# Kernel optimization log

Measured on AMD Instinct MI355X. Metric: run time of the kernel, lower is better.

## Reference

```python
import jax, jax.numpy as jnp
import numpy as np

N_SRC = 100000
N_DST = 20000
E = 1250000
D_IN = 64
D_OUT = 64
NEG_SLOPE = 0.2  # PyG GATConv default


def setup_inputs() -> dict:
    key = jax.random.key(0)
    ks = jax.random.split(key, 8)
    x = jax.random.normal(ks[0], (N_SRC, D_IN), dtype=jnp.float32)
    res_n_id = jax.random.randint(ks[1], (N_DST,), 0, N_SRC)
    edge_src = jax.random.randint(ks[2], (E,), 0, N_SRC)
    edge_dst = jax.random.randint(ks[3], (E,), 0, N_DST)
    W = jax.random.normal(ks[4], (D_IN, D_OUT), dtype=jnp.float32) / np.sqrt(D_IN)
    att_src = jax.random.normal(ks[5], (D_OUT,), dtype=jnp.float32)
    att_dst = jax.random.normal(ks[6], (D_OUT,), dtype=jnp.float32)
    bias = jax.random.normal(ks[7], (D_OUT,), dtype=jnp.float32) * 0.01
    return {"x": x, "res_n_id": res_n_id, "edge_src": edge_src,
            "edge_dst": edge_dst, "W": W, "att_src": att_src,
            "att_dst": att_dst, "bias": bias}


def reference(x, res_n_id, edge_src, edge_dst, W, att_src, att_dst, bias):
    # Shared linear transform (in_channels is an int -> one weight in PyG)
    h_src = x @ W                      # [N_src, D_OUT]
    h_dst = x[res_n_id] @ W            # [N_dst, D_OUT]
    # Per-node attention logits
    a_src = h_src @ att_src            # [N_src]
    a_dst = h_dst @ att_dst            # [N_dst]
    # Per-edge attention score (gather)
    e = jax.nn.leaky_relu(a_src[edge_src] + a_dst[edge_dst], NEG_SLOPE)  # [E]
    # Segment softmax over incoming edges of each destination node
    m = jax.ops.segment_max(e, edge_dst, num_segments=N_DST)             # [N_dst]
    ex = jnp.exp(e - m[edge_dst])
    denom = jax.ops.segment_sum(ex, edge_dst, num_segments=N_DST)        # [N_dst]
    alpha = ex / (denom[edge_dst] + 1e-16)                               # [E]
    # (dropout on alpha is eval-mode identity)
    # Weighted scatter-aggregate
    msg = h_src[edge_src] * alpha[:, None]                               # [E, D_OUT]
    out = jax.ops.segment_sum(msg, edge_dst, num_segments=N_DST)         # [N_dst, D_OUT]
    return out + bias
```

## Files before the change

### kernel.cpp

```cpp
#include <hip/hip_runtime.h>

#define N_SRC 100000
#define N_DST 20000
#define NE    1250000
#define D     64
#define NEG_SLOPE 0.2f

#define NBKT 1250
#define BCAP 1536
#define TILE 4096

__device__ __forceinline__ unsigned short f2bf(float f) {
    unsigned u = __float_as_uint(f);
    u += 0x7FFFu + ((u >> 16) & 1);
    return (unsigned short)(u >> 16);
}
__device__ __forceinline__ float blo(unsigned u) { return __uint_as_float(u << 16); }
__device__ __forceinline__ float bhi(unsigned u) { return __uint_as_float(u & 0xFFFF0000u); }

__global__ void k_wad_init(const float* __restrict__ W,
                           const float* __restrict__ att_dst,
                           float* __restrict__ wad, int* __restrict__ gcur) {
    int g = blockIdx.x * 256 + threadIdx.x;
    if (g < NBKT) gcur[g] = g * BCAP;
    if (g < D) {
        float s = 0.f;
#pragma unroll
        for (int c = 0; c < D; ++c) s += W[g * D + c] * att_dst[c];
        wad[g] = s;
    }
}

__global__ __launch_bounds__(256) void k_h(const float* __restrict__ x,
                                           const float* __restrict__ W,
                                           const float* __restrict__ att_src,
                                           unsigned short* __restrict__ hb,
                                           float* __restrict__ a_src) {
    __shared__ float xs[64 * 68];
    __shared__ float Ws[64 * 64];
    int t = threadIdx.x;
    int row0 = blockIdx.x * 64;
    int nrows = N_SRC - row0; if (nrows > 64) nrows = 64;
    {
        const float4* W4 = (const float4*)W;
        float4* Ws4 = (float4*)Ws;
#pragma unroll
        for (int p = 0; p < 4; ++p) Ws4[t + 256 * p] = W4[t + 256 * p];
    }
#pragma unroll
    for (int p = 0; p < 4; ++p) {
        int idx = t + 256 * p;
        int r = idx >> 4, kq = idx & 15;
        float4 v = make_float4(0.f, 0.f, 0.f, 0.f);
        if (r < nrows) v = *(const float4*)(x + (size_t)(row0 + r) * D + 4 * kq);
        xs[(4 * kq + 0) * 68 + r] = v.x;
        xs[(4 * kq + 1) * 68 + r] = v.y;
        xs[(4 * kq + 2) * 68 + r] = v.z;
        xs[(4 * kq + 3) * 68 + r] = v.w;
    }
    __syncthreads();
    int ry = t >> 4, cx = t & 15;
    float acc[4][4] = {{0.f}};
#pragma unroll 8
    for (int k = 0; k < 64; ++k) {
        float4 xv = *(const float4*)(xs + k * 68 + 4 * ry);
        float4 wv = *(const float4*)(Ws + k * 64 + 4 * cx);
        acc[0][0] = fmaf(xv.x, wv.x, acc[0][0]); acc[0][1] = fmaf(xv.x, wv.y, acc[0][1]);
        acc[0][2] = fmaf(xv.x, wv.z, acc[0][2]); acc[0][3] = fmaf(xv.x, wv.w, acc[0][3]);
        acc[1][0] = fmaf(xv.y, wv.x, acc[1][0]); acc[1][1] = fmaf(xv.y, wv.y, acc[1][1]);
        acc[1][2] = fmaf(xv.y, wv.z, acc[1][2]); acc[1][3] = fmaf(xv.y, wv.w, acc[1][3]);
        acc[2][0] = fmaf(xv.z, wv.x, acc[2][0]); acc[2][1] = fmaf(xv.z, wv.y, acc[2][1]);
        acc[2][2] = fmaf(xv.z, wv.z, acc[2][2]); acc[2][3] = fmaf(xv.z, wv.w, acc[2][3]);
        acc[3][0] = fmaf(xv.w, wv.x, acc[3][0]); acc[3][1] = fmaf(xv.w, wv.y, acc[3][1]);
        acc[3][2] = fmaf(xv.w, wv.z, acc[3][2]); acc[3][3] = fmaf(xv.w, wv.w, acc[3][3]);
    }
    float4 a4 = *(const float4*)(att_src + 4 * cx);
#pragma unroll
    for (int j = 0; j < 4; ++j) {
        int r = 4 * ry + j;
        if (r < nrows) {
            ushort4 hv;
            hv.x = f2bf(acc[j][0]); hv.y = f2bf(acc[j][1]);
            hv.z = f2bf(acc[j][2]); hv.w = f2bf(acc[j][3]);
            *(ushort4*)(hb + (size_t)(row0 + r) * D + 4 * cx) = hv;
        }
        float p = acc[j][0] * a4.x + acc[j][1] * a4.y + acc[j][2] * a4.z + acc[j][3] * a4.w;
        p += __shfl_xor(p, 1, 64); p += __shfl_xor(p, 2, 64);
        p += __shfl_xor(p, 4, 64); p += __shfl_xor(p, 8, 64);
        if (cx == 0 && r < nrows) a_src[row0 + r] = p;
    }
}

__global__ __launch_bounds__(256) void k_adst(const float* __restrict__ x,
                                              const int* __restrict__ res_n_id,
                                              const float* __restrict__ wad,
                                              float* __restrict__ a_dst) {
    int tid = threadIdx.x;
    int wid = blockIdx.x * 4 + (tid >> 6);
    int lane = tid & 63;
    if (wid >= N_DST) return;
    int row = res_n_id[wid];
    float p = x[(size_t)row * D + lane] * wad[lane];
#pragma unroll
    for (int off = 32; off; off >>= 1) p += __shfl_xor(p, off, 64);
    if (lane == 0) a_dst[wid] = p;
}

__global__ __launch_bounds__(1024) void k_bucket(const int* __restrict__ es,
                                                 const int* __restrict__ ed,
                                                 int* __restrict__ gcur,
                                                 int* __restrict__ buf) {
    __shared__ int hist[NBKT];
    __shared__ int lofs[NBKT];
    __shared__ int gbase[NBKT];
    __shared__ int wtot[16];
    __shared__ int stage[TILE];
    int t = threadIdx.x;
    int w = t >> 6, lane = t & 63;
    int base = blockIdx.x * TILE;
    int nE = NE - base; if (nE > TILE) nE = TILE;

    for (int i = t; i < NBKT; i += 1024) hist[i] = 0;
    __syncthreads();

    int s_[4], d_[4], rk_[4];
#pragma unroll
    for (int j = 0; j < 4; ++j) {
        int i = t + 1024 * j;
        d_[j] = -1;
        if (i < nE) {
            s_[j] = es[base + i];
            d_[j] = ed[base + i];
            rk_[j] = atomicAdd(&hist[d_[j] >> 4], 1);
        }
    }
    __syncthreads();

    int c0 = t * 2;
    int h0 = 0, h1 = 0;
    if (c0 < NBKT) { h0 = hist[c0]; h1 = hist[c0 + 1]; }
    int sum = h0 + h1;
    int incl = sum;
#pragma unroll
    for (int off = 1; off < 64; off <<= 1) {
        int u = __shfl_up(incl, off, 64);
        if (lane >= off) incl += u;
    }
    if (lane == 63) wtot[w] = incl;
    __syncthreads();
    int wpre = 0;
#pragma unroll
    for (int j = 0; j < 16; ++j) wpre += (j < w) ? wtot[j] : 0;
    if (c0 < NBKT) {
        int run = wpre + incl - sum;
        lofs[c0] = run;
        gbase[c0] = h0 ? atomicAdd(&gcur[c0], h0) : 0;
        run += h0;
        lofs[c0 + 1] = run;
        gbase[c0 + 1] = h1 ? atomicAdd(&gcur[c0 + 1], h1) : 0;
    }
    __syncthreads();

#pragma unroll
    for (int j = 0; j < 4; ++j) {
        if (d_[j] >= 0) {
            int b = d_[j] >> 4;
            stage[lofs[b] + rk_[j]] = s_[j] | ((d_[j] & 15) << 17) | (b << 21);
        }
    }
    __syncthreads();

    for (int idx = t; idx < nE; idx += 1024) {
        int rec = stage[idx];
        int b = ((unsigned)rec) >> 21;
        int gpos = gbase[b] + idx - lofs[b];
        if (gpos < (b + 1) * BCAP) buf[gpos] = rec;
    }
}

__global__ __launch_bounds__(512) void k_aggB(const int* __restrict__ buf,
                                              const int* __restrict__ gcur,
                                              const float* __restrict__ a_src,
                                              const float* __restrict__ a_dst,
                                              const unsigned short* __restrict__ hb,
                                              const float* __restrict__ bias,
                                              float* __restrict__ out) {
    __shared__ int2 sorted[BCAP];
    __shared__ int  scw[16 * 8];
    __shared__ int  begs[17];
    int bk = blockIdx.x;
    int t = threadIdx.x;
    int w = t >> 6, lane = t & 63;
    int n = gcur[bk] - bk * BCAP;
    if (n > BCAP) n = BCAP;
    if (n < 0) n = 0;

    const int* src = buf + (size_t)bk * BCAP;
    int r0 = 0, r1 = 0, r2 = 0;
    int bin0 = -1, bin1 = -1, bin2 = -1;
    if (t < n)        { r0 = src[t];        bin0 = (r0 >> 17) & 15; }
    if (t + 512 < n)  { r1 = src[t + 512];  bin1 = (r1 >> 17) & 15; }
    if (t + 1024 < n) { r2 = src[t + 1024]; bin2 = (r2 >> 17) & 15; }

    int h[16], incl[16];
#pragma unroll
    for (int i = 0; i < 16; ++i)
        h[i] = (bin0 == i) + (bin1 == i) + (bin2 == i);

#pragma unroll
    for (int i = 0; i < 16; ++i) {
        int v = h[i];
#pragma unroll
        for (int off = 1; off < 64; off <<= 1) {
            int u = __shfl_up(v, off, 64);
            if (lane >= off) v += u;
        }
        incl[i] = v;
        int tot = __shfl(v, 63, 64);
        if (lane == 0) scw[i * 8 + w] = tot;
    }
    __syncthreads();

    for (int off = 1; off < 128; off <<= 1) {
        int up = 0;
        if (t < 128 && t >= off) up = scw[t - off];
        __syncthreads();
        if (t < 128 && t >= off) scw[t] += up;
        __syncthreads();
    }
    if (t < 16) begs[t] = (t == 0) ? 0 : scw[t * 8 - 1];
    if (t == 16) begs[16] = n;

    int p0 = 0, p1 = 0, p2 = 0;
#pragma unroll
    for (int i = 0; i < 16; ++i) {
        int idx = i * 8 + w;
        int base_i = ((idx ? scw[idx - 1] : 0)) + (incl[i] - h[i]);
        p0 += (bin0 == i) ? base_i : 0;
        p1 += (bin1 == i) ? base_i : 0;
        p2 += (bin2 == i) ? base_i : 0;
    }
    p1 += (bin1 == bin0);
    p2 += (bin2 == bin0) + (bin2 == bin1);
    if (bin0 >= 0) sorted[p0].x = r0;
    if (bin1 >= 0) sorted[p1].x = r1;
    if (bin2 >= 0) sorted[p2].x = r2;
    __syncthreads();

    int g = lane >> 3, il = lane & 7;
    float4 bA = *(const float4*)(bias + 8 * il);
    float4 bB = *(const float4*)(bias + 8 * il + 4);
#pragma unroll
    for (int q = 0; q < 2; ++q) {
        int dlo = w * 2 + q;
        int beg = begs[dlo], end = begs[dlo + 1];
        float ad = a_dst[bk * 16 + dlo];

        float mx = -1e30f;
        for (int i = beg + lane; i < end; i += 64) {
            int meta = sorted[i].x;
            float v = a_src[meta & 0x1FFFF] + ad;
            v = v > 0.f ? v : NEG_SLOPE * v;
            sorted[i].y = __float_as_int(v);
            mx = fmaxf(mx, v);
        }
#pragma unroll
        for (int off = 32; off; off >>= 1) mx = fmaxf(mx, __shfl_xor(mx, off, 64));
        __builtin_amdgcn_wave_barrier();

        float a0 = 0.f, a1 = 0.f, a2 = 0.f, a3 = 0.f;
        float a4c = 0.f, a5 = 0.f, a6 = 0.f, a7 = 0.f;
        float den = 0.f;
        int i = beg;
        for (; i + 16 <= end; i += 16) {
            int2 ra = sorted[i + g];
            int2 rb = sorted[i + 8 + g];
            const uint4 ha = *(const uint4*)(hb + (size_t)(ra.x & 0x1FFFF) * D + 8 * il);
            const uint4 hc = *(const uint4*)(hb + (size_t)(rb.x & 0x1FFFF) * D + 8 * il);
            float ea = __expf(__int_as_float(ra.y) - mx);
            float eb = __expf(__int_as_float(rb.y) - mx);
            a0 = fmaf(ea, blo(ha.x), a0); a1 = fmaf(ea, bhi(ha.x), a1);
            a2 = fmaf(ea, blo(ha.y), a2); a3 = fmaf(ea, bhi(ha.y), a3);
            a4c = fmaf(ea, blo(ha.z), a4c); a5 = fmaf(ea, bhi(ha.z), a5);
            a6 = fmaf(ea, blo(ha.w), a6); a7 = fmaf(ea, bhi(ha.w), a7);
            a0 = fmaf(eb, blo(hc.x), a0); a1 = fmaf(eb, bhi(hc.x), a1);
            a2 = fmaf(eb, blo(hc.y), a2); a3 = fmaf(eb, bhi(hc.y), a3);
            a4c = fmaf(eb, blo(hc.z), a4c); a5 = fmaf(eb, bhi(hc.z), a5);
            a6 = fmaf(eb, blo(hc.w), a6); a7 = fmaf(eb, bhi(hc.w), a7);
            den += ea + eb;
        }
        for (; i < end; i += 8) {
            int idx = i + g;
            bool ok = idx < end;
            float e = 0.f;
            if (ok) {
                int2 r = sorted[idx];
                e = __expf(__int_as_float(r.y) - mx);
                const uint4 hv = *(const uint4*)(hb + (size_t)(r.x & 0x1FFFF) * D + 8 * il);
                a0 = fmaf(e, blo(hv.x), a0); a1 = fmaf(e, bhi(hv.x), a1);
                a2 = fmaf(e, blo(hv.y), a2); a3 = fmaf(e, bhi(hv.y), a3);
                a4c = fmaf(e, blo(hv.z), a4c); a5 = fmaf(e, bhi(hv.z), a5);
                a6 = fmaf(e, blo(hv.w), a6); a7 = fmaf(e, bhi(hv.w), a7);
            }
            den += e;
        }
#pragma unroll
        for (int off = 8; off <= 32; off <<= 1) {
            a0 += __shfl_xor(a0, off, 64); a1 += __shfl_xor(a1, off, 64);
            a2 += __shfl_xor(a2, off, 64); a3 += __shfl_xor(a3, off, 64);
            a4c += __shfl_xor(a4c, off, 64); a5 += __shfl_xor(a5, off, 64);
            a6 += __shfl_xor(a6, off, 64); a7 += __shfl_xor(a7, off, 64);
            den += __shfl_xor(den, off, 64);
        }
        if (g == 0) {
            float inv = 1.f / (den + 1e-16f);
            float4 oA, oB;
            oA.x = a0 * inv + bA.x; oA.y = a1 * inv + bA.y;
            oA.z = a2 * inv + bA.z; oA.w = a3 * inv + bA.w;
            oB.x = a4c * inv + bB.x; oB.y = a5 * inv + bB.y;
            oB.z = a6 * inv + bB.z; oB.w = a7 * inv + bB.w;
            float* orow = out + ((size_t)bk * 16 + dlo) * D + 8 * il;
            *(float4*)orow = oA;
            *(float4*)(orow + 4) = oB;
        }
    }
}

extern "C" void kernel_launch(void* const* d_in, const int* in_sizes, int n_in,
                              void* d_out, int out_size, void* d_ws, size_t ws_size,
                              hipStream_t stream) {
    const float* x        = (const float*)d_in[0];
    const int*   res_n_id = (const int*)d_in[1];
    const int*   edge_src = (const int*)d_in[2];
    const int*   edge_dst = (const int*)d_in[3];
    const float* W        = (const float*)d_in[4];
    const float* att_src  = (const float*)d_in[5];
    const float* att_dst  = (const float*)d_in[6];
    const float* bias     = (const float*)d_in[7];
    float* out = (float*)d_out;

    char* w = (char*)d_ws;
    unsigned short* hb = (unsigned short*)w; w += (size_t)N_SRC * D * 2;
    int*   buf   = (int*)w;   w += (size_t)NBKT * BCAP * 4;
    float* a_src = (float*)w; w += (size_t)N_SRC * 4;
    float* a_dst = (float*)w; w += (size_t)N_DST * 4;
    float* wad   = (float*)w; w += 256;
    int*   gcur  = (int*)w;   w += (size_t)NBKT * 4;

    k_wad_init<<<(NBKT + 255) / 256, 256, 0, stream>>>(W, att_dst, wad, gcur);
    k_h<<<(N_SRC + 63) / 64, 256, 0, stream>>>(x, W, att_src, hb, a_src);
    k_adst<<<N_DST / 4, 256, 0, stream>>>(x, res_n_id, wad, a_dst);
    k_bucket<<<(NE + TILE - 1) / TILE, 1024, 0, stream>>>(edge_src, edge_dst, gcur, buf);
    k_aggB<<<NBKT, 512, 0, stream>>>(buf, gcur, a_src, a_dst, hb, bias, out);
}
```

Measured before the change: 168.3 us.

## Halve bucket size, fuse a_dst computation into aggregation, unroll gather by four

Buckets now hold 8 destination nodes instead of 16 (2500 buckets, capacity 768), and the aggregation kernel runs with 256 threads per block. The separate a_dst kernel is removed; each wave computes its destination's attention logit inline from x, res_n_id and wad, which saves one launch and one global round-trip. The block-level scan now uses a single-wave shuffle scan instead of a multi-barrier shared-memory scan. A 32-edge unrolled loop adds more independent gathers in flight, at the cost of more registers and smaller per-bucket capacity margins for overflow.

Measured after the change: 161.3 us. 4.2% less time.

```diff
diff --git a/kernel.cpp b/kernel.cpp
--- a/kernel.cpp
+++ b/kernel.cpp
@@ -6,8 +6,8 @@
 #define D     64
 #define NEG_SLOPE 0.2f
 
-#define NBKT 1250
-#define BCAP 1536
+#define NBKT 2500
+#define BCAP 768
 #define TILE 4096
 
 __device__ __forceinline__ unsigned short f2bf(float f) {
@@ -91,21 +91,6 @@
     }
 }
 
-__global__ __launch_bounds__(256) void k_adst(const float* __restrict__ x,
-                                              const int* __restrict__ res_n_id,
-                                              const float* __restrict__ wad,
-                                              float* __restrict__ a_dst) {
-    int tid = threadIdx.x;
-    int wid = blockIdx.x * 4 + (tid >> 6);
-    int lane = tid & 63;
-    if (wid >= N_DST) return;
-    int row = res_n_id[wid];
-    float p = x[(size_t)row * D + lane] * wad[lane];
-#pragma unroll
-    for (int off = 32; off; off >>= 1) p += __shfl_xor(p, off, 64);
-    if (lane == 0) a_dst[wid] = p;
-}
-
 __global__ __launch_bounds__(1024) void k_bucket(const int* __restrict__ es,
                                                  const int* __restrict__ ed,
                                                  int* __restrict__ gcur,
@@ -131,15 +116,17 @@
         if (i < nE) {
             s_[j] = es[base + i];
             d_[j] = ed[base + i];
-            rk_[j] = atomicAdd(&hist[d_[j] >> 4], 1);
-        }
-    }
-    __syncthreads();
-
-    int c0 = t * 2;
-    int h0 = 0, h1 = 0;
-    if (c0 < NBKT) { h0 = hist[c0]; h1 = hist[c0 + 1]; }
-    int sum = h0 + h1;
+            rk_[j] = atomicAdd(&hist[d_[j] >> 3], 1);
+        }
+    }
+    __syncthreads();
+
+    int c0 = t * 3;
+    int hc[3] = {0, 0, 0};
+#pragma unroll
+    for (int j = 0; j < 3; ++j)
+        if (c0 + j < NBKT) hc[j] = hist[c0 + j];
+    int sum = hc[0] + hc[1] + hc[2];
     int incl = sum;
 #pragma unroll
     for (int off = 1; off < 64; off <<= 1) {
@@ -151,43 +138,49 @@
     int wpre = 0;
 #pragma unroll
     for (int j = 0; j < 16; ++j) wpre += (j < w) ? wtot[j] : 0;
-    if (c0 < NBKT) {
+    {
         int run = wpre + incl - sum;
-        lofs[c0] = run;
-        gbase[c0] = h0 ? atomicAdd(&gcur[c0], h0) : 0;
-        run += h0;
-        lofs[c0 + 1] = run;
-        gbase[c0 + 1] = h1 ? atomicAdd(&gcur[c0 + 1], h1) : 0;
+#pragma unroll
+        for (int j = 0; j < 3; ++j) {
+            int b = c0 + j;
+            if (b < NBKT) {
+                lofs[b] = run;
+                gbase[b] = hc[j] ? atomicAdd(&gcur[b], hc[j]) : 0;
+                run += hc[j];
+            }
+        }
     }
     __syncthreads();
 
 #pragma unroll
     for (int j = 0; j < 4; ++j) {
         if (d_[j] >= 0) {
-            int b = d_[j] >> 4;
-            stage[lofs[b] + rk_[j]] = s_[j] | ((d_[j] & 15) << 17) | (b << 21);
+            int b = d_[j] >> 3;
+            stage[lofs[b] + rk_[j]] = s_[j] | ((d_[j] & 7) << 17) | (b << 20);
         }
     }
     __syncthreads();
 
     for (int idx = t; idx < nE; idx += 1024) {
         int rec = stage[idx];
-        int b = ((unsigned)rec) >> 21;
+        int b = ((unsigned)rec) >> 20;
         int gpos = gbase[b] + idx - lofs[b];
         if (gpos < (b + 1) * BCAP) buf[gpos] = rec;
     }
 }
 
-__global__ __launch_bounds__(512) void k_aggB(const int* __restrict__ buf,
+__global__ __launch_bounds__(256) void k_aggB(const int* __restrict__ buf,
                                               const int* __restrict__ gcur,
                                               const float* __restrict__ a_src,
-                                              const float* __restrict__ a_dst,
+                                              const float* __restrict__ x,
+                                              const int* __restrict__ res_n_id,
+                                              const float* __restrict__ wad,
                                               const unsigned short* __restrict__ hb,
                                               const float* __restrict__ bias,
                                               float* __restrict__ out) {
     __shared__ int2 sorted[BCAP];
-    __shared__ int  scw[16 * 8];
-    __shared__ int  begs[17];
+    __shared__ int  scw[8 * 4];
+    __shared__ int  begs[9];
     int bk = blockIdx.x;
     int t = threadIdx.x;
     int w = t >> 6, lane = t & 63;
@@ -198,17 +191,17 @@
     const int* src = buf + (size_t)bk * BCAP;
     int r0 = 0, r1 = 0, r2 = 0;
     int bin0 = -1, bin1 = -1, bin2 = -1;
-    if (t < n)        { r0 = src[t];        bin0 = (r0 >> 17) & 15; }
-    if (t + 512 < n)  { r1 = src[t + 512];  bin1 = (r1 >> 17) & 15; }
-    if (t + 1024 < n) { r2 = src[t + 1024]; bin2 = (r2 >> 17) & 15; }
-
-    int h[16], incl[16];
-#pragma unroll
-    for (int i = 0; i < 16; ++i)
+    if (t < n)       { r0 = src[t];       bin0 = (r0 >> 17) & 7; }
+    if (t + 256 < n) { r1 = src[t + 256]; bin1 = (r1 >> 17) & 7; }
+    if (t + 512 < n) { r2 = src[t + 512]; bin2 = (r2 >> 17) & 7; }
+
+    int h[8], incl[8];
+#pragma unroll
+    for (int i = 0; i < 8; ++i)
         h[i] = (bin0 == i) + (bin1 == i) + (bin2 == i);
 
 #pragma unroll
-    for (int i = 0; i < 16; ++i) {
+    for (int i = 0; i < 8; ++i) {
         int v = h[i];
 #pragma unroll
         for (int off = 1; off < 64; off <<= 1) {
@@ -217,24 +210,27 @@
         }
         incl[i] = v;
         int tot = __shfl(v, 63, 64);
-        if (lane == 0) scw[i * 8 + w] = tot;
-    }
-    __syncthreads();
-
-    for (int off = 1; off < 128; off <<= 1) {
-        int up = 0;
-        if (t < 128 && t >= off) up = scw[t - off];
-        __syncthreads();
-        if (t < 128 && t >= off) scw[t] += up;
-        __syncthreads();
-    }
-    if (t < 16) begs[t] = (t == 0) ? 0 : scw[t * 8 - 1];
-    if (t == 16) begs[16] = n;
+        if (lane == 0) scw[i * 4 + w] = tot;
+    }
+    __syncthreads();
+
+    if (t < 32) {
+        int v = scw[t];
+#pragma unroll
+        for (int off = 1; off < 32; off <<= 1) {
+            int u = __shfl_up(v, off, 64);
+            if (t >= off) v += u;
+        }
+        scw[t] = v;
+    }
+    __syncthreads();
+    if (t < 8) begs[t] = (t == 0) ? 0 : scw[t * 4 - 1];
+    if (t == 8) begs[8] = n;
 
     int p0 = 0, p1 = 0, p2 = 0;
 #pragma unroll
-    for (int i = 0; i < 16; ++i) {
-        int idx = i * 8 + w;
+    for (int i = 0; i < 8; ++i) {
+        int idx = i * 4 + w;
         int base_i = ((idx ? scw[idx - 1] : 0)) + (incl[i] - h[i]);
         p0 += (bin0 == i) ? base_i : 0;
         p1 += (bin1 == i) ? base_i : 0;
@@ -245,6 +241,7 @@
     if (bin0 >= 0) sorted[p0].x = r0;
     if (bin1 >= 0) sorted[p1].x = r1;
     if (bin2 >= 0) sorted[p2].x = r2;
+    float wv = wad[lane];
     __syncthreads();
 
     int g = lane >> 3, il = lane & 7;
@@ -254,7 +251,11 @@
     for (int q = 0; q < 2; ++q) {
         int dlo = w * 2 + q;
         int beg = begs[dlo], end = begs[dlo + 1];
-        float ad = a_dst[bk * 16 + dlo];
+
+        int xrow = res_n_id[bk * 8 + dlo];
+        float ad = x[(size_t)xrow * D + lane] * wv;
+#pragma unroll
+        for (int off = 32; off; off >>= 1) ad += __shfl_xor(ad, off, 64);
 
         float mx = -1e30f;
         for (int i = beg + lane; i < end; i += 64) {
@@ -272,21 +273,52 @@
         float a4c = 0.f, a5 = 0.f, a6 = 0.f, a7 = 0.f;
         float den = 0.f;
         int i = beg;
+        for (; i + 32 <= end; i += 32) {
+            int2 ra = sorted[i + g];
+            int2 rb = sorted[i + 8 + g];
+            int2 rc = sorted[i + 16 + g];
+            int2 rd = sorted[i + 24 + g];
+            const uint4 ha = *(const uint4*)(hb + (size_t)(ra.x & 0x1FFFF) * D + 8 * il);
+            const uint4 hc4 = *(const uint4*)(hb + (size_t)(rb.x & 0x1FFFF) * D + 8 * il);
+            const uint4 he = *(const uint4*)(hb + (size_t)(rc.x & 0x1FFFF) * D + 8 * il);
+            const uint4 hf = *(const uint4*)(hb + (size_t)(rd.x & 0x1FFFF) * D + 8 * il);
+            float ea = __expf(__int_as_float(ra.y) - mx);
+            float eb = __expf(__int_as_float(rb.y) - mx);
+            float ec = __expf(__int_as_float(rc.y) - mx);
+            float ed = __expf(__int_as_float(rd.y) - mx);
+            a0 = fmaf(ea, blo(ha.x), a0); a1 = fmaf(ea, bhi(ha.x), a1);
+            a2 = fmaf(ea, blo(ha.y), a2); a3 = fmaf(ea, bhi(ha.y), a3);
+            a4c = fmaf(ea, blo(ha.z), a4c); a5 = fmaf(ea, bhi(ha.z), a5);
+            a6 = fmaf(ea, blo(ha.w), a6); a7 = fmaf(ea, bhi(ha.w), a7);
+            a0 = fmaf(eb, blo(hc4.x), a0); a1 = fmaf(eb, bhi(hc4.x), a1);
+            a2 = fmaf(eb, blo(hc4.y), a2); a3 = fmaf(eb, bhi(hc4.y), a3);
+            a4c = fmaf(eb, blo(hc4.z), a4c); a5 = fmaf(eb, bhi(hc4.z), a5);
+            a6 = fmaf(eb, blo(hc4.w), a6); a7 = fmaf(eb, bhi(hc4.w), a7);
+            a0 = fmaf(ec, blo(he.x), a0); a1 = fmaf(ec, bhi(he.x), a1);
+            a2 = fmaf(ec, blo(he.y), a2); a3 = fmaf(ec, bhi(he.y), a3);
+            a4c = fmaf(ec, blo(he.z), a4c); a5 = fmaf(ec, bhi(he.z), a5);
+            a6 = fmaf(ec, blo(he.w), a6); a7 = fmaf(ec, bhi(he.w), a7);
+            a0 = fmaf(ed, blo(hf.x), a0); a1 = fmaf(ed, bhi(hf.x), a1);
+            a2 = fmaf(ed, blo(hf.y), a2); a3 = fmaf(ed, bhi(hf.y), a3);
+            a4c = fmaf(ed, blo(hf.z), a4c); a5 = fmaf(ed, bhi(hf.z), a5);
+            a6 = fmaf(ed, blo(hf.w), a6); a7 = fmaf(ed, bhi(hf.w), a7);
+            den += (ea + eb) + (ec + ed);
+        }
         for (; i + 16 <= end; i += 16) {
             int2 ra = sorted[i + g];
             int2 rb = sorted[i + 8 + g];
             const uint4 ha = *(const uint4*)(hb + (size_t)(ra.x & 0x1FFFF) * D + 8 * il);
-            const uint4 hc = *(const uint4*)(hb + (size_t)(rb.x & 0x1FFFF) * D + 8 * il);
+            const uint4 hc4 = *(const uint4*)(hb + (size_t)(rb.x & 0x1FFFF) * D + 8 * il);
             float ea = __expf(__int_as_float(ra.y) - mx);
             float eb = __expf(__int_as_float(rb.y) - mx);
             a0 = fmaf(ea, blo(ha.x), a0); a1 = fmaf(ea, bhi(ha.x), a1);
             a2 = fmaf(ea, blo(ha.y), a2); a3 = fmaf(ea, bhi(ha.y), a3);
             a4c = fmaf(ea, blo(ha.z), a4c); a5 = fmaf(ea, bhi(ha.z), a5);
             a6 = fmaf(ea, blo(ha.w), a6); a7 = fmaf(ea, bhi(ha.w), a7);
-            a0 = fmaf(eb, blo(hc.x), a0); a1 = fmaf(eb, bhi(hc.x), a1);
-            a2 = fmaf(eb, blo(hc.y), a2); a3 = fmaf(eb, bhi(hc.y), a3);
-            a4c = fmaf(eb, blo(hc.z), a4c); a5 = fmaf(eb, bhi(hc.z), a5);
-            a6 = fmaf(eb, blo(hc.w), a6); a7 = fmaf(eb, bhi(hc.w), a7);
+            a0 = fmaf(eb, blo(hc4.x), a0); a1 = fmaf(eb, bhi(hc4.x), a1);
+            a2 = fmaf(eb, blo(hc4.y), a2); a3 = fmaf(eb, bhi(hc4.y), a3);
+            a4c = fmaf(eb, blo(hc4.z), a4c); a5 = fmaf(eb, bhi(hc4.z), a5);
+            a6 = fmaf(eb, blo(hc4.w), a6); a7 = fmaf(eb, bhi(hc4.w), a7);
             den += ea + eb;
         }
         for (; i < end; i += 8) {
@@ -319,7 +351,7 @@
             oA.z = a2 * inv + bA.z; oA.w = a3 * inv + bA.w;
             oB.x = a4c * inv + bB.x; oB.y = a5 * inv + bB.y;
             oB.z = a6 * inv + bB.z; oB.w = a7 * inv + bB.w;
-            float* orow = out + ((size_t)bk * 16 + dlo) * D + 8 * il;
+            float* orow = out + ((size_t)bk * 8 + dlo) * D + 8 * il;
             *(float4*)orow = oA;
             *(float4*)(orow + 4) = oB;
         }
@@ -343,13 +375,11 @@
     unsigned short* hb = (unsigned short*)w; w += (size_t)N_SRC * D * 2;
     int*   buf   = (int*)w;   w += (size_t)NBKT * BCAP * 4;
     float* a_src = (float*)w; w += (size_t)N_SRC * 4;
-    float* a_dst = (float*)w; w += (size_t)N_DST * 4;
     float* wad   = (float*)w; w += 256;
     int*   gcur  = (int*)w;   w += (size_t)NBKT * 4;
 
     k_wad_init<<<(NBKT + 255) / 256, 256, 0, stream>>>(W, att_dst, wad, gcur);
     k_h<<<(N_SRC + 63) / 64, 256, 0, stream>>>(x, W, att_src, hb, a_src);
-    k_adst<<<N_DST / 4, 256, 0, stream>>>(x, res_n_id, wad, a_dst);
     k_bucket<<<(NE + TILE - 1) / TILE, 1024, 0, stream>>>(edge_src, edge_dst, gcur, buf);
-    k_aggB<<<NBKT, 512, 0, stream>>>(buf, gcur, a_src, a_dst, hb, bias, out);
-}
+    k_aggB<<<NBKT, 256, 0, stream>>>(buf, gcur, a_src, x, res_n_id, wad, hb, bias, out);
+}
```
